# Performance work log

Measured on AMD Instinct MI355X. Metric: run time of the kernel, lower is better.

## Reference

```python
import jax, jax.numpy as jnp
import numpy as np

B, N, IN_DIM, OUT_DIM = 8, 2048, 128, 64
TEMPERATURE = 1.0
NEG_SLOPE = 0.2


def setup_inputs() -> dict:
    key = jax.random.key(0)
    k1, k2, k3, k4, k5 = jax.random.split(key, 5)
    s_fc = 1.0 / np.sqrt(IN_DIM)
    s_at = 1.0 / np.sqrt(2 * OUT_DIM)
    return {
        "h": jax.random.normal(k1, (B, N, IN_DIM), dtype=jnp.float32),
        "W_fc": jax.random.normal(k2, (IN_DIM, OUT_DIM), dtype=jnp.float32) * s_fc,
        "b_fc": jax.random.normal(k3, (OUT_DIM,), dtype=jnp.float32) * s_fc,
        "a_src": jax.random.normal(k4, (OUT_DIM,), dtype=jnp.float32) * s_at,
        "a_dst": jax.random.normal(k5, (OUT_DIM,), dtype=jnp.float32) * s_at,
        "b_attn": jnp.zeros((), dtype=jnp.float32),
    }


def reference(h, W_fc, b_fc, a_src, a_dst, b_attn):
    # hp: (B, N, OUT_DIM) -- projected node features
    hp = h @ W_fc + b_fc
    # attn_fc(concat(h_i, h_j)) == h_i@a_src + h_j@a_dst + b (exact decomposition)
    s = hp @ a_src  # (B, N) source contribution
    d = hp @ a_dst  # (B, N) dest contribution
    scores = s[:, :, None] + d[:, None, :] + b_attn  # (B, N, N)
    scores = jnp.where(scores >= 0, scores, NEG_SLOPE * scores)  # leaky_relu
    scores = scores / TEMPERATURE
    attn = jax.nn.softmax(scores, axis=-1)
    out = jnp.einsum("bij,bjd->bid", attn, hp)
    return jax.nn.elu(out)
```

## Files before the change

### kernel.cpp

```cpp
#include <hip/hip_runtime.h>
#include <hip/hip_bf16.h>
#include <math.h>

#define BB 8
#define NN 2048
#define IND 128
#define OUTD 64
#define NEG 0.2f

typedef __attribute__((ext_vector_type(8))) short short8;
typedef __attribute__((ext_vector_type(4))) float f32x4;

__device__ __forceinline__ unsigned short f2bf(float f) {
    unsigned int u = __float_as_uint(f);
    u += 0x7fffu + ((u >> 16) & 1u);
    return (unsigned short)(u >> 16);
}

__device__ __forceinline__ unsigned int pk_bf16(float a, float b) {
    union { __hip_bfloat162 h; unsigned int u; } cv;
    cv.h = __float22bfloat162_rn(make_float2(a, b));
    return cv.u;
}

__global__ __launch_bounds__(256) void gat_proj_kernel(
    const float* __restrict__ h, const float* __restrict__ W,
    const float* __restrict__ bfc, const float* __restrict__ asrc,
    const float* __restrict__ adst,
    unsigned short* __restrict__ hpT2, float* __restrict__ s,
    float* __restrict__ d)
{
    __shared__ float Wl[IND * OUTD];
    __shared__ float hl[64 * 132];

    const int t  = threadIdx.x;
    const int R0 = blockIdx.x * 64;

    const float4* W4 = (const float4*)W;
    float4*       Wl4 = (float4*)Wl;
    #pragma unroll
    for (int k2 = 0; k2 < 8; ++k2) Wl4[t + k2 * 256] = W4[t + k2 * 256];

    const float4* h4 = (const float4*)(h + (size_t)R0 * IND);
    #pragma unroll
    for (int k2 = 0; k2 < 8; ++k2) {
        const int idx = t + k2 * 256;
        const int row = idx >> 5, c4 = idx & 31;
        *(float4*)&hl[row * 132 + c4 * 4] = h4[idx];
    }
    __syncthreads();

    const int r0 = (t >> 4) * 4;
    const int o0 = (t & 15) * 4;
    const float4 bias = *(const float4*)(bfc + o0);
    float4 a0 = bias, a1 = bias, a2 = bias, a3 = bias;

    #pragma unroll 4
    for (int k = 0; k < IND; ++k) {
        const float4 w4 = *(const float4*)&Wl[k * OUTD + o0];
        const float h0 = hl[(r0 + 0) * 132 + k];
        const float h1 = hl[(r0 + 1) * 132 + k];
        const float h2 = hl[(r0 + 2) * 132 + k];
        const float h3 = hl[(r0 + 3) * 132 + k];
        a0.x = fmaf(h0, w4.x, a0.x); a0.y = fmaf(h0, w4.y, a0.y);
        a0.z = fmaf(h0, w4.z, a0.z); a0.w = fmaf(h0, w4.w, a0.w);
        a1.x = fmaf(h1, w4.x, a1.x); a1.y = fmaf(h1, w4.y, a1.y);
        a1.z = fmaf(h1, w4.z, a1.z); a1.w = fmaf(h1, w4.w, a1.w);
        a2.x = fmaf(h2, w4.x, a2.x); a2.y = fmaf(h2, w4.y, a2.y);
        a2.z = fmaf(h2, w4.z, a2.z); a2.w = fmaf(h2, w4.w, a2.w);
        a3.x = fmaf(h3, w4.x, a3.x); a3.y = fmaf(h3, w4.y, a3.y);
        a3.z = fmaf(h3, w4.z, a3.z); a3.w = fmaf(h3, w4.w, a3.w);
    }

    const int b   = R0 >> 11;
    const int jb0 = (R0 & 2047) + r0;
    const int cj  = jb0 >> 3;
    const int sub = jb0 & 7;
    unsigned short* cbase = hpT2 + (((size_t)(b * 256 + cj)) * OUTD) * 8;
    {
        ushort4 v;
        v.x = f2bf(a0.x); v.y = f2bf(a1.x); v.z = f2bf(a2.x); v.w = f2bf(a3.x);
        *(ushort4*)(cbase + (o0 + 0) * 8 + sub) = v;
        v.x = f2bf(a0.y); v.y = f2bf(a1.y); v.z = f2bf(a2.y); v.w = f2bf(a3.y);
        *(ushort4*)(cbase + (o0 + 1) * 8 + sub) = v;
        v.x = f2bf(a0.z); v.y = f2bf(a1.z); v.z = f2bf(a2.z); v.w = f2bf(a3.z);
        *(ushort4*)(cbase + (o0 + 2) * 8 + sub) = v;
        v.x = f2bf(a0.w); v.y = f2bf(a1.w); v.z = f2bf(a2.w); v.w = f2bf(a3.w);
        *(ushort4*)(cbase + (o0 + 3) * 8 + sub) = v;
    }

    const float4 as4 = *(const float4*)(asrc + o0);
    const float4 ad4 = *(const float4*)(adst + o0);
    float vs[4], vd[4];
    vs[0] = a0.x*as4.x + a0.y*as4.y + a0.z*as4.z + a0.w*as4.w;
    vs[1] = a1.x*as4.x + a1.y*as4.y + a1.z*as4.z + a1.w*as4.w;
    vs[2] = a2.x*as4.x + a2.y*as4.y + a2.z*as4.z + a2.w*as4.w;
    vs[3] = a3.x*as4.x + a3.y*as4.y + a3.z*as4.z + a3.w*as4.w;
    vd[0] = a0.x*ad4.x + a0.y*ad4.y + a0.z*ad4.z + a0.w*ad4.w;
    vd[1] = a1.x*ad4.x + a1.y*ad4.y + a1.z*ad4.z + a1.w*ad4.w;
    vd[2] = a2.x*ad4.x + a2.y*ad4.y + a2.z*ad4.z + a2.w*ad4.w;
    vd[3] = a3.x*ad4.x + a3.y*ad4.y + a3.z*ad4.z + a3.w*ad4.w;
    #pragma unroll
    for (int msk = 1; msk <= 8; msk <<= 1) {
        #pragma unroll
        for (int r = 0; r < 4; ++r) {
            vs[r] += __shfl_xor(vs[r], msk);
            vd[r] += __shfl_xor(vd[r], msk);
        }
    }
    if ((t & 15) == 0) {
        #pragma unroll
        for (int r = 0; r < 4; ++r) {
            s[R0 + r0 + r] = vs[r];
            d[R0 + r0 + r] = vd[r];
        }
    }
}

__global__ __launch_bounds__(256) void gat_attn_kernel(
    const unsigned short* __restrict__ hpT2, const float* __restrict__ s,
    const float* __restrict__ d, const float* __restrict__ battn_p,
    float* __restrict__ out)
{
    __shared__ float accl[4][16 * 65];
    __shared__ float ll[4][16];

    const int t    = threadIdx.x;
    const int lane = t & 63;
    const int wv   = t >> 6;
    const int tile = blockIdx.x;
    const int b    = tile >> 7;
    const int i0   = (tile & 127) * 16;
    const int m    = lane & 15;
    const int kc   = lane >> 4;

    const float battn = battn_p[0];
    const float* db   = d + b * NN;
    const float  sm   = s[b * NN + i0 + m] + battn;
    const unsigned short* hb = hpT2 + (size_t)b * 256 * OUTD * 8;

    f32x4 acc0 = {0.f, 0.f, 0.f, 0.f};
    f32x4 acc1 = {0.f, 0.f, 0.f, 0.f};
    f32x4 acc2 = {0.f, 0.f, 0.f, 0.f};
    f32x4 acc3 = {0.f, 0.f, 0.f, 0.f};
    float l = 0.f;

    const int jbase = wv * (NN / 4);

    #pragma unroll 2
    for (int it = 0; it < NN / 4 / 32; ++it) {
        const int j0 = jbase + it * 32;
        const float4 da  = *(const float4*)(db + j0 + kc * 8);
        const float4 dbv = *(const float4*)(db + j0 + kc * 8 + 4);
        float wf[8];
        {
            float x;
            x = sm + da.x;  wf[0] = __expf(fmaxf(x, NEG * x));
            x = sm + da.y;  wf[1] = __expf(fmaxf(x, NEG * x));
            x = sm + da.z;  wf[2] = __expf(fmaxf(x, NEG * x));
            x = sm + da.w;  wf[3] = __expf(fmaxf(x, NEG * x));
            x = sm + dbv.x; wf[4] = __expf(fmaxf(x, NEG * x));
            x = sm + dbv.y; wf[5] = __expf(fmaxf(x, NEG * x));
            x = sm + dbv.z; wf[6] = __expf(fmaxf(x, NEG * x));
            x = sm + dbv.w; wf[7] = __expf(fmaxf(x, NEG * x));
        }
        l += ((wf[0] + wf[1]) + (wf[2] + wf[3])) +
             ((wf[4] + wf[5]) + (wf[6] + wf[7]));

        union { short8 s8; unsigned int u[4]; } af;
        af.u[0] = pk_bf16(wf[0], wf[1]);
        af.u[1] = pk_bf16(wf[2], wf[3]);
        af.u[2] = pk_bf16(wf[4], wf[5]);
        af.u[3] = pk_bf16(wf[6], wf[7]);

        const size_t cb = ((size_t)((j0 >> 3) + kc)) * OUTD * 8;
        const short8 bf0 = *(const short8*)(hb + cb + (0 * 16 + m) * 8);
        const short8 bf1 = *(const short8*)(hb + cb + (1 * 16 + m) * 8);
        const short8 bf2 = *(const short8*)(hb + cb + (2 * 16 + m) * 8);
        const short8 bf3 = *(const short8*)(hb + cb + (3 * 16 + m) * 8);

        acc0 = __builtin_amdgcn_mfma_f32_16x16x32_bf16(af.s8, bf0, acc0, 0, 0, 0);
        acc1 = __builtin_amdgcn_mfma_f32_16x16x32_bf16(af.s8, bf1, acc1, 0, 0, 0);
        acc2 = __builtin_amdgcn_mfma_f32_16x16x32_bf16(af.s8, bf2, acc2, 0, 0, 0);
        acc3 = __builtin_amdgcn_mfma_f32_16x16x32_bf16(af.s8, bf3, acc3, 0, 0, 0);
    }

    l += __shfl_xor(l, 16);
    l += __shfl_xor(l, 32);
    if (kc == 0) ll[wv][m] = l;

    #pragma unroll
    for (int r = 0; r < 4; ++r) {
        const int row = kc * 4 + r;
        accl[wv][row * 65 + 0 * 16 + m] = acc0[r];
        accl[wv][row * 65 + 1 * 16 + m] = acc1[r];
        accl[wv][row * 65 + 2 * 16 + m] = acc2[r];
        accl[wv][row * 65 + 3 * 16 + m] = acc3[r];
    }
    __syncthreads();

    const int col = t & 63;
    const int r0e = (t >> 6) * 4;
    float* ob = out + (((size_t)b * NN + i0) * OUTD);
    #pragma unroll
    for (int r = 0; r < 4; ++r) {
        const int row = r0e + r;
        const float lsum = (ll[0][row] + ll[1][row]) + (ll[2][row] + ll[3][row]);
        float v = (accl[0][row * 65 + col] + accl[1][row * 65 + col]) +
                  (accl[2][row * 65 + col] + accl[3][row * 65 + col]);
        v /= lsum;
        v = (v > 0.f) ? v : expm1f(v);
        ob[(size_t)row * OUTD + col] = v;
    }
}

extern "C" void kernel_launch(void* const* d_in, const int* in_sizes, int n_in,
                              void* d_out, int out_size, void* d_ws, size_t ws_size,
                              hipStream_t stream)
{
    const float* h     = (const float*)d_in[0];
    const float* W     = (const float*)d_in[1];
    const float* bfc   = (const float*)d_in[2];
    const float* asrc  = (const float*)d_in[3];
    const float* adst  = (const float*)d_in[4];
    const float* battn = (const float*)d_in[5];
    float* out = (float*)d_out;

    unsigned short* hpT2 = (unsigned short*)d_ws;
    float* s = (float*)((char*)d_ws + (size_t)BB * NN * OUTD * 2);
    float* d = s + (size_t)BB * NN;

    gat_proj_kernel<<<(BB * NN) / 64, 256, 0, stream>>>(h, W, bfc, asrc, adst,
                                                        hpT2, s, d);
    gat_attn_kernel<<<BB * NN / 16, 256, 0, stream>>>(hpT2, s, d, battn, out);
}
```

Before: 91.92 us.

## Factor leaky-relu exponentials into per-node terms and compute row sums via MFMA

Uses exp(leaky(s+d)) = max(exp(s)exp(d), exp(0.2s)exp(0.2d)) to precompute exp(d) and exp(0.2d) per node in the projection kernel. The attention inner loop then does two multiplies and a max per element instead of an exp. The softmax denominator is computed with an extra MFMA against a ones vector rather than scalar adds and shuffles. The projection kernel also switches to float4 LDS reads of h with a 4-wide k step. The risks are overflow or underflow, since there is no max subtraction and large s or d could give inf or 0 where the original exponent of the sum was fine, plus one extra H array read per element.

```diff
diff --git a/kernel.cpp b/kernel.cpp
--- a/kernel.cpp
+++ b/kernel.cpp
@@ -28,7 +28,7 @@
     const float* __restrict__ bfc, const float* __restrict__ asrc,
     const float* __restrict__ adst,
     unsigned short* __restrict__ hpT2, float* __restrict__ s,
-    float* __restrict__ d)
+    float* __restrict__ F, float* __restrict__ H)
 {
     __shared__ float Wl[IND * OUTD];
     __shared__ float hl[64 * 132];
@@ -55,21 +55,52 @@
     const float4 bias = *(const float4*)(bfc + o0);
     float4 a0 = bias, a1 = bias, a2 = bias, a3 = bias;
 
-    #pragma unroll 4
-    for (int k = 0; k < IND; ++k) {
-        const float4 w4 = *(const float4*)&Wl[k * OUTD + o0];
-        const float h0 = hl[(r0 + 0) * 132 + k];
-        const float h1 = hl[(r0 + 1) * 132 + k];
-        const float h2 = hl[(r0 + 2) * 132 + k];
-        const float h3 = hl[(r0 + 3) * 132 + k];
-        a0.x = fmaf(h0, w4.x, a0.x); a0.y = fmaf(h0, w4.y, a0.y);
-        a0.z = fmaf(h0, w4.z, a0.z); a0.w = fmaf(h0, w4.w, a0.w);
-        a1.x = fmaf(h1, w4.x, a1.x); a1.y = fmaf(h1, w4.y, a1.y);
-        a1.z = fmaf(h1, w4.z, a1.z); a1.w = fmaf(h1, w4.w, a1.w);
-        a2.x = fmaf(h2, w4.x, a2.x); a2.y = fmaf(h2, w4.y, a2.y);
-        a2.z = fmaf(h2, w4.z, a2.z); a2.w = fmaf(h2, w4.w, a2.w);
-        a3.x = fmaf(h3, w4.x, a3.x); a3.y = fmaf(h3, w4.y, a3.y);
-        a3.z = fmaf(h3, w4.z, a3.z); a3.w = fmaf(h3, w4.w, a3.w);
+    #pragma unroll 2
+    for (int kc = 0; kc < IND; kc += 4) {
+        const float4 w0 = *(const float4*)&Wl[(kc + 0) * OUTD + o0];
+        const float4 w1 = *(const float4*)&Wl[(kc + 1) * OUTD + o0];
+        const float4 w2 = *(const float4*)&Wl[(kc + 2) * OUTD + o0];
+        const float4 w3 = *(const float4*)&Wl[(kc + 3) * OUTD + o0];
+        const float4 h0 = *(const float4*)&hl[(r0 + 0) * 132 + kc];
+        const float4 h1 = *(const float4*)&hl[(r0 + 1) * 132 + kc];
+        const float4 h2 = *(const float4*)&hl[(r0 + 2) * 132 + kc];
+        const float4 h3 = *(const float4*)&hl[(r0 + 3) * 132 + kc];
+
+        a0.x = fmaf(h0.x, w0.x, a0.x); a0.y = fmaf(h0.x, w0.y, a0.y);
+        a0.z = fmaf(h0.x, w0.z, a0.z); a0.w = fmaf(h0.x, w0.w, a0.w);
+        a0.x = fmaf(h0.y, w1.x, a0.x); a0.y = fmaf(h0.y, w1.y, a0.y);
+        a0.z = fmaf(h0.y, w1.z, a0.z); a0.w = fmaf(h0.y, w1.w, a0.w);
+        a0.x = fmaf(h0.z, w2.x, a0.x); a0.y = fmaf(h0.z, w2.y, a0.y);
+        a0.z = fmaf(h0.z, w2.z, a0.z); a0.w = fmaf(h0.z, w2.w, a0.w);
+        a0.x = fmaf(h0.w, w3.x, a0.x); a0.y = fmaf(h0.w, w3.y, a0.y);
+        a0.z = fmaf(h0.w, w3.z, a0.z); a0.w = fmaf(h0.w, w3.w, a0.w);
+
+        a1.x = fmaf(h1.x, w0.x, a1.x); a1.y = fmaf(h1.x, w0.y, a1.y);
+        a1.z = fmaf(h1.x, w0.z, a1.z); a1.w = fmaf(h1.x, w0.w, a1.w);
+        a1.x = fmaf(h1.y, w1.x, a1.x); a1.y = fmaf(h1.y, w1.y, a1.y);
+        a1.z = fmaf(h1.y, w1.z, a1.z); a1.w = fmaf(h1.y, w1.w, a1.w);
+        a1.x = fmaf(h1.z, w2.x, a1.x); a1.y = fmaf(h1.z, w2.y, a1.y);
+        a1.z = fmaf(h1.z, w2.z, a1.z); a1.w = fmaf(h1.z, w2.w, a1.w);
+        a1.x = fmaf(h1.w, w3.x, a1.x); a1.y = fmaf(h1.w, w3.y, a1.y);
+        a1.z = fmaf(h1.w, w3.z, a1.z); a1.w = fmaf(h1.w, w3.w, a1.w);
+
+        a2.x = fmaf(h2.x, w0.x, a2.x); a2.y = fmaf(h2.x, w0.y, a2.y);
+        a2.z = fmaf(h2.x, w0.z, a2.z); a2.w = fmaf(h2.x, w0.w, a2.w);
+        a2.x = fmaf(h2.y, w1.x, a2.x); a2.y = fmaf(h2.y, w1.y, a2.y);
+        a2.z = fmaf(h2.y, w1.z, a2.z); a2.w = fmaf(h2.y, w1.w, a2.w);
+        a2.x = fmaf(h2.z, w2.x, a2.x); a2.y = fmaf(h2.z, w2.y, a2.y);
+        a2.z = fmaf(h2.z, w2.z, a2.z); a2.w = fmaf(h2.z, w2.w, a2.w);
+        a2.x = fmaf(h2.w, w3.x, a2.x); a2.y = fmaf(h2.w, w3.y, a2.y);
+        a2.z = fmaf(h2.w, w3.z, a2.z); a2.w = fmaf(h2.w, w3.w, a2.w);
+
+        a3.x = fmaf(h3.x, w0.x, a3.x); a3.y = fmaf(h3.x, w0.y, a3.y);
+        a3.z = fmaf(h3.x, w0.z, a3.z); a3.w = fmaf(h3.x, w0.w, a3.w);
+        a3.x = fmaf(h3.y, w1.x, a3.x); a3.y = fmaf(h3.y, w1.y, a3.y);
+        a3.z = fmaf(h3.y, w1.z, a3.z); a3.w = fmaf(h3.y, w1.w, a3.w);
+        a3.x = fmaf(h3.z, w2.x, a3.x); a3.y = fmaf(h3.z, w2.y, a3.y);
+        a3.z = fmaf(h3.z, w2.z, a3.z); a3.w = fmaf(h3.z, w2.w, a3.w);
+        a3.x = fmaf(h3.w, w3.x, a3.x); a3.y = fmaf(h3.w, w3.y, a3.y);
+        a3.z = fmaf(h3.w, w3.z, a3.z); a3.w = fmaf(h3.w, w3.w, a3.w);
     }
 
     const int b   = R0 >> 11;
@@ -112,15 +143,16 @@
         #pragma unroll
         for (int r = 0; r < 4; ++r) {
             s[R0 + r0 + r] = vs[r];
-            d[R0 + r0 + r] = vd[r];
+            F[R0 + r0 + r] = __expf(vd[r]);
+            H[R0 + r0 + r] = __expf(NEG * vd[r]);
         }
     }
 }
 
 __global__ __launch_bounds__(256) void gat_attn_kernel(
     const unsigned short* __restrict__ hpT2, const float* __restrict__ s,
-    const float* __restrict__ d, const float* __restrict__ battn_p,
-    float* __restrict__ out)
+    const float* __restrict__ F, const float* __restrict__ H,
+    const float* __restrict__ battn_p, float* __restrict__ out)
 {
     __shared__ float accl[4][16 * 65];
     __shared__ float ll[4][16];
@@ -135,37 +167,41 @@
     const int kc   = lane >> 4;
 
     const float battn = battn_p[0];
-    const float* db   = d + b * NN;
-    const float  sm   = s[b * NN + i0 + m] + battn;
+    const float sm = s[b * NN + i0 + m] + battn;
+    const float Ei = __expf(sm);
+    const float Gi = __expf(NEG * sm);
+    const float* Fb = F + b * NN;
+    const float* Hb = H + b * NN;
     const unsigned short* hb = hpT2 + (size_t)b * 256 * OUTD * 8;
+
+    short8 ones;
+    #pragma unroll
+    for (int q = 0; q < 8; ++q) ones[q] = (short)0x3F80;
 
     f32x4 acc0 = {0.f, 0.f, 0.f, 0.f};
     f32x4 acc1 = {0.f, 0.f, 0.f, 0.f};
     f32x4 acc2 = {0.f, 0.f, 0.f, 0.f};
     f32x4 acc3 = {0.f, 0.f, 0.f, 0.f};
-    float l = 0.f;
+    f32x4 accl4 = {0.f, 0.f, 0.f, 0.f};
 
     const int jbase = wv * (NN / 4);
 
     #pragma unroll 2
     for (int it = 0; it < NN / 4 / 32; ++it) {
         const int j0 = jbase + it * 32;
-        const float4 da  = *(const float4*)(db + j0 + kc * 8);
-        const float4 dbv = *(const float4*)(db + j0 + kc * 8 + 4);
+        const float4 Fa = *(const float4*)(Fb + j0 + kc * 8);
+        const float4 Fc = *(const float4*)(Fb + j0 + kc * 8 + 4);
+        const float4 Ha = *(const float4*)(Hb + j0 + kc * 8);
+        const float4 Hc = *(const float4*)(Hb + j0 + kc * 8 + 4);
         float wf[8];
-        {
-            float x;
-            x = sm + da.x;  wf[0] = __expf(fmaxf(x, NEG * x));
-            x = sm + da.y;  wf[1] = __expf(fmaxf(x, NEG * x));
-            x = sm + da.z;  wf[2] = __expf(fmaxf(x, NEG * x));
-            x = sm + da.w;  wf[3] = __expf(fmaxf(x, NEG * x));
-            x = sm + dbv.x; wf[4] = __expf(fmaxf(x, NEG * x));
-            x = sm + dbv.y; wf[5] = __expf(fmaxf(x, NEG * x));
-            x = sm + dbv.z; wf[6] = __expf(fmaxf(x, NEG * x));
-            x = sm + dbv.w; wf[7] = __expf(fmaxf(x, NEG * x));
-        }
-        l += ((wf[0] + wf[1]) + (wf[2] + wf[3])) +
-             ((wf[4] + wf[5]) + (wf[6] + wf[7]));
+        wf[0] = fmaxf(Ei * Fa.x, Gi * Ha.x);
+        wf[1] = fmaxf(Ei * Fa.y, Gi * Ha.y);
+        wf[2] = fmaxf(Ei * Fa.z, Gi * Ha.z);
+        wf[3] = fmaxf(Ei * Fa.w, Gi * Ha.w);
+        wf[4] = fmaxf(Ei * Fc.x, Gi * Hc.x);
+        wf[5] = fmaxf(Ei * Fc.y, Gi * Hc.y);
+        wf[6] = fmaxf(Ei * Fc.z, Gi * Hc.z);
+        wf[7] = fmaxf(Ei * Fc.w, Gi * Hc.w);
 
         union { short8 s8; unsigned int u[4]; } af;
         af.u[0] = pk_bf16(wf[0], wf[1]);
@@ -183,11 +219,13 @@
         acc1 = __builtin_amdgcn_mfma_f32_16x16x32_bf16(af.s8, bf1, acc1, 0, 0, 0);
         acc2 = __builtin_amdgcn_mfma_f32_16x16x32_bf16(af.s8, bf2, acc2, 0, 0, 0);
         acc3 = __builtin_amdgcn_mfma_f32_16x16x32_bf16(af.s8, bf3, acc3, 0, 0, 0);
-    }
-
-    l += __shfl_xor(l, 16);
-    l += __shfl_xor(l, 32);
-    if (kc == 0) ll[wv][m] = l;
+        accl4 = __builtin_amdgcn_mfma_f32_16x16x32_bf16(af.s8, ones, accl4, 0, 0, 0);
+    }
+
+    if (m == 0) {
+        #pragma unroll
+        for (int r = 0; r < 4; ++r) ll[wv][kc * 4 + r] = accl4[r];
+    }
 
     #pragma unroll
     for (int r = 0; r < 4; ++r) {
@@ -228,9 +266,10 @@
 
     unsigned short* hpT2 = (unsigned short*)d_ws;
     float* s = (float*)((char*)d_ws + (size_t)BB * NN * OUTD * 2);
-    float* d = s + (size_t)BB * NN;
+    float* F = s + (size_t)BB * NN;
+    float* H = F + (size_t)BB * NN;
 
     gat_proj_kernel<<<(BB * NN) / 64, 256, 0, stream>>>(h, W, bfc, asrc, adst,
-                                                        hpT2, s, d);
-    gat_attn_kernel<<<BB * NN / 16, 256, 0, stream>>>(hpT2, s, d, battn, out);
-}
+                                                        hpT2, s, F, H);
+    gat_attn_kernel<<<BB * NN / 16, 256, 0, stream>>>(hpT2, s, F, H, battn, out);
+}
```

After: 93.45 us. No clear change (+1.7%).
